# Optimization experiments

Hardware: AMD Instinct MI355X
Metric: run time of the kernel (lower is better)

Reference implementation:

```python
import jax, jax.numpy as jnp
import numpy as np

SCALING_FACTOR = 128.0


def setup_inputs() -> dict:
    key = jax.random.key(0)
    k1, k2, k3, k4 = jax.random.split(key, 4)
    B, G1, G2, DX, DZ, NT = 4, 128, 128, 2, 128, 2048
    x_grid = jax.random.uniform(k1, (B, G1, G2, DX), dtype=jnp.float32)
    z_grid = jax.random.normal(k2, (B, G1, G2, DZ), dtype=jnp.float32)
    xt = jax.random.uniform(k3, (B, NT, DX), dtype=jnp.float32)
    # raw (pre-softplus) lengthscale parameter, one per input dim
    init_ls = 0.1
    lengthscale_param = jnp.full((DX,), np.log(np.exp(init_ls) - 1.0), dtype=jnp.float32)
    lengthscale_param = lengthscale_param + 0.01 * jax.random.normal(k4, (DX,), dtype=jnp.float32)
    return {"x_grid": x_grid, "z_grid": z_grid, "xt": xt, "lengthscale_param": lengthscale_param}


def reference(x_grid, z_grid, xt, lengthscale_param):
    B = x_grid.shape[0]
    dx = x_grid.shape[-1]
    dz = z_grid.shape[-1]
    # flatten spatial grid dims -> (B, ng, d)
    xg = x_grid.reshape(B, -1, dx)
    zg = z_grid.reshape(B, -1, dz)
    # lengthscale = 1e-5 + softplus(param), shape (dx,)
    ls = 1e-5 + jax.nn.softplus(lengthscale_param)
    # pairwise scaled squared distances: (B, nt, ng)
    diff = (xt[:, :, None, :] - xg[:, None, :, :]) / ls  # (B, nt, ng, dx)
    dist2 = jnp.sum(diff * diff, axis=-1)
    weights = jnp.exp(-0.5 * dist2)  # (B, nt, ng)
    # weighted smoothing onto targets
    out = jnp.einsum("btg,bgz->btz", weights, zg) / SCALING_FACTOR
    return out
```

## Files before the change

kernel.cpp:

```cpp
#include <hip/hip_runtime.h>
#include <hip/hip_bf16.h>
#include <cstdint>
#include <cstddef>


typedef float  f32x4  __attribute__((ext_vector_type(4)));
typedef float  f32x16 __attribute__((ext_vector_type(16)));
typedef short  short8 __attribute__((ext_vector_type(8)));
typedef unsigned short ushort4v __attribute__((ext_vector_type(4)));
typedef unsigned short ushort8 __attribute__((ext_vector_type(8)));

#if __has_builtin(__builtin_amdgcn_exp2f)
#define EXP2F(x) __builtin_amdgcn_exp2f(x)
#else
#define EXP2F(x) exp2f(x)
#endif

#define AS1C(p) ((const __attribute__((address_space(1))) void*)(p))
#define AS3(p)  ((__attribute__((address_space(3))) void*)(p))

__device__ __forceinline__ unsigned short bf16_bits(float f) {
  __bf16 h = (__bf16)f;
  return __builtin_bit_cast(unsigned short, h);
}

__global__ __launch_bounds__(256) void pre_kernel(
    const float* __restrict__ x_grid, const float* __restrict__ z_grid,
    const float* __restrict__ xt, const float* __restrict__ lsp,
    unsigned short* __restrict__ zgb, float* __restrict__ xg_trip,
    float* __restrict__ xt4)
{
  __shared__ unsigned short lt[64 * 128];
  const int bid = blockIdx.x;
  const int b   = bid >> 8;
  const int grp = bid & 255;
  const int tid = threadIdx.x;
  const size_t gbase = (size_t)b * 16384 + grp * 64;
  const float sc = 1.0f / 128.0f;

  const float* zr = z_grid + gbase * 128;
  #pragma unroll
  for (int it = 0; it < 8; ++it) {
    const int idx = it * 256 + tid;
    const int row = idx >> 5, c4 = idx & 31;
    f32x4 v = *(const f32x4*)(zr + row * 128 + c4 * 4);
    ushort4v o;
    o.x = bf16_bits(v.x * sc); o.y = bf16_bits(v.y * sc);
    o.z = bf16_bits(v.z * sc); o.w = bf16_bits(v.w * sc);
    *(ushort4v*)(lt + row * 128 + c4 * 4) = o;
  }

  if (tid < 128) {
    const float ls0 = 1e-5f + log1pf(expf(lsp[0]));
    const float ls1 = 1e-5f + log1pf(expf(lsp[1]));
    const float cs  = sqrtf(0.7213475204444817f);
    const float s0 = cs / ls0, s1 = cs / ls1;
    if (tid < 64) {
      const size_t g = gbase + tid;
      const float u0 = x_grid[g * 2 + 0] * s0;
      const float u1 = x_grid[g * 2 + 1] * s1;
      float* d = xg_trip + g * 3;
      d[0] = 2.0f * u0; d[1] = 2.0f * u1; d[2] = -(u0 * u0 + u1 * u1);
    } else if (bid < 128) {
      const int bx = bid >> 5;
      const int r  = (bid & 31) * 64 + (tid - 64);
      const float u0 = xt[((size_t)(bx * 2048 + r)) * 2 + 0] * s0;
      const float u1 = xt[((size_t)(bx * 2048 + r)) * 2 + 1] * s1;
      f32x4 d; d.x = u0; d.y = u1; d.z = -(u0 * u0 + u1 * u1); d.w = 0.0f;
      *(f32x4*)(xt4 + ((size_t)(bx * 2048 + r)) * 4) = d;
    }
  }

  __syncthreads();

  const int q2p = tid >> 7, c = tid & 127;
  #pragma unroll
  for (int h = 0; h < 4; ++h) {
    ushort8 o;
    #pragma unroll
    for (int hi = 0; hi < 2; ++hi)
      #pragma unroll
      for (int j = 0; j < 4; ++j)
        o[hi * 4 + j] = lt[(h * 16 + 4 * q2p + 8 * hi + j) * 128 + c];
    *(ushort8*)(zgb + ((size_t)(b * 1024 + grp * 4 + h)) * 2048
                    + (size_t)(q2p * 128 + c) * 8) = o;
  }
}

__global__ __launch_bounds__(256, 2) void main_kernel(
    const unsigned short* __restrict__ zgb,
    const float* __restrict__ xg_trip,
    const float* __restrict__ xt4,
    float* __restrict__ out,
    float* __restrict__ partials)
{
  __shared__ __align__(128) char smem[65536];
  char* ring = smem;
  char* trip = smem + 24576;

  const int raw = blockIdx.x;
  const int lid = (raw & 7) * 64 + (raw >> 3);
  const int mt  = lid & 15;
  const int b   = (lid >> 4) & 3;
  const int ksp = lid >> 6;

  const int tid = threadIdx.x;
  const int wv  = tid >> 6;
  const int l   = tid & 63;
  const int rh  = wv & 1;
  const int kk  = wv >> 1;
  const int l31 = l & 31;
  const int q2  = l >> 5;
  const int chunk = ksp * 2 + kk;

  float at0[2], at1[2], ca[2];
  #pragma unroll
  for (int mi = 0; mi < 2; ++mi) {
    const int r = mt * 128 + rh * 64 + mi * 32 + l31;
    f32x4 v = *(const f32x4*)(xt4 + ((size_t)(b * 2048 + r)) * 4);
    at0[mi] = v.x; at1[mi] = v.y; ca[mi] = v.z;
  }

  f32x16 acc[2][4];
  #pragma unroll
  for (int mi = 0; mi < 2; ++mi)
    #pragma unroll
    for (int ni = 0; ni < 4; ++ni)
      #pragma unroll
      for (int e = 0; e < 16; ++e)
        acc[mi][ni][e] = 0.0f;

  const char* zsrc = (const char*)zgb + ((size_t)(b * 1024 + chunk * 64)) * 4096;
  const char* tsrc = (const char*)xg_trip + ((size_t)(b * 16384 + ksp * 2048)) * 12;

  auto stage = [&](int s) {
    const char* zs = zsrc + (size_t)s * 4096 + rh * 2048;
    char* zd = ring + (s % 3) * 8192 + kk * 4096 + rh * 2048;
    __builtin_amdgcn_global_load_lds(AS1C(zs + l * 16), AS3(zd + l * 16), 16, 0, 0);
    __builtin_amdgcn_global_load_lds(AS1C(zs + 1024 + l * 16),
                                     AS3(zd + 1024 + l * 16), 16, 0, 0);
  };

  #pragma unroll
  for (int w = 0; w < 6; ++w) {
    const int off = wv * 6144 + w * 1024 + l * 16;
    __builtin_amdgcn_global_load_lds(AS1C(tsrc + off), AS3(trip + off), 16, 0, 0);
  }
  stage(0);
  stage(1);

  #pragma unroll 3
  for (int s = 0; s < 64; ++s) {
    if (s < 63) { asm volatile("s_waitcnt vmcnt(2)" ::: "memory"); }
    else        { asm volatile("s_waitcnt vmcnt(0)" ::: "memory"); }
    __builtin_amdgcn_s_barrier();
    asm volatile("" ::: "memory");

    if (s + 2 < 64) stage(s + 2);

    const float* tb = (const float*)(trip + kk * 12288 + s * 192 + q2 * 48);
    f32x4 L0 = *(const f32x4*)(tb + 0);
    f32x4 L1 = *(const f32x4*)(tb + 4);
    f32x4 L2 = *(const f32x4*)(tb + 8);
    f32x4 H0 = *(const f32x4*)(tb + 24);
    f32x4 H1 = *(const f32x4*)(tb + 28);
    f32x4 H2 = *(const f32x4*)(tb + 32);
    float g0[8], g1[8], cb[8];
    g0[0]=L0.x; g1[0]=L0.y; cb[0]=L0.z;
    g0[1]=L0.w; g1[1]=L1.x; cb[1]=L1.y;
    g0[2]=L1.z; g1[2]=L1.w; cb[2]=L2.x;
    g0[3]=L2.y; g1[3]=L2.z; cb[3]=L2.w;
    g0[4]=H0.x; g1[4]=H0.y; cb[4]=H0.z;
    g0[5]=H0.w; g1[5]=H1.x; cb[5]=H1.y;
    g0[6]=H1.z; g1[6]=H1.w; cb[6]=H2.x;
    g0[7]=H2.y; g1[7]=H2.z; cb[7]=H2.w;

    const char* zt = ring + (s % 3) * 8192 + kk * 4096 + q2 * 2048 + l31 * 16;
    short8 bfr[4];
    #pragma unroll
    for (int ni = 0; ni < 4; ++ni)
      bfr[ni] = *(const short8*)(zt + ni * 512);

    short8 af[2];
    #pragma unroll
    for (int mi = 0; mi < 2; ++mi) {
      union { short8 s8; __bf16 e[8]; } u;
      #pragma unroll
      for (int j = 0; j < 8; ++j) {
        float arg = __builtin_fmaf(at0[mi], g0[j],
                    __builtin_fmaf(at1[mi], g1[j], ca[mi] + cb[j]));
        u.e[j] = (__bf16)EXP2F(arg);
      }
      af[mi] = u.s8;
    }

    #pragma unroll
    for (int mi = 0; mi < 2; ++mi)
      #pragma unroll
      for (int ni = 0; ni < 4; ++ni)
        acc[mi][ni] = __builtin_amdgcn_mfma_f32_32x32x16_bf16(
            af[mi], bfr[ni], acc[mi][ni], 0, 0, 0);
  }

  __syncthreads();
  if (kk == 1) {
    #pragma unroll
    for (int mi = 0; mi < 2; ++mi)
      #pragma unroll
      for (int ni = 0; ni < 4; ++ni)
        #pragma unroll
        for (int q = 0; q < 4; ++q) {
          f32x4 v;
          v.x = acc[mi][ni][q * 4 + 0]; v.y = acc[mi][ni][q * 4 + 1];
          v.z = acc[mi][ni][q * 4 + 2]; v.w = acc[mi][ni][q * 4 + 3];
          *(f32x4*)(smem + rh * 32768 + (mi * 4 + ni) * 4096 + q * 1024 + l * 16) = v;
        }
  }
  __syncthreads();
  if (kk == 0) {
    float* pb = partials ? partials + ((size_t)(ksp * 64 + b * 16 + mt)) * 16384
                         : nullptr;
    #pragma unroll
    for (int mi = 0; mi < 2; ++mi)
      #pragma unroll
      for (int ni = 0; ni < 4; ++ni) {
        #pragma unroll
        for (int q = 0; q < 4; ++q) {
          f32x4 v = *(const f32x4*)(smem + rh * 32768 + (mi * 4 + ni) * 4096
                                         + q * 1024 + l * 16);
          acc[mi][ni][q * 4 + 0] += v.x; acc[mi][ni][q * 4 + 1] += v.y;
          acc[mi][ni][q * 4 + 2] += v.z; acc[mi][ni][q * 4 + 3] += v.w;
        }
        #pragma unroll
        for (int r = 0; r < 16; ++r) {
          const int row = rh * 64 + mi * 32
                        + (r & 3) + 8 * (r >> 2) + 4 * q2;
          const int col = ni * 32 + l31;
          if (pb) {
            pb[row * 128 + col] = acc[mi][ni][r];
          } else {
            atomicAdd(out + ((size_t)b * 2048 + mt * 128 + row) * 128 + col,
                      acc[mi][ni][r]);
          }
        }
      }
  }
}

__global__ __launch_bounds__(256) void reduce_kernel(
    const float* __restrict__ partials, float* __restrict__ out)
{
  const size_t base = ((size_t)blockIdx.x * 256 + threadIdx.x) * 4;
  const float* p = partials + base;
  f32x4 s = *(const f32x4*)p;
  #pragma unroll
  for (int ksv = 1; ksv < 8; ++ksv) {
    f32x4 v = *(const f32x4*)(p + (size_t)ksv * 1048576);
    s.x += v.x; s.y += v.y; s.z += v.z; s.w += v.w;
  }
  *(f32x4*)(out + base) = s;
}

extern "C" void kernel_launch(void* const* d_in, const int* in_sizes, int n_in,
                              void* d_out, int out_size, void* d_ws, size_t ws_size,
                              hipStream_t stream) {
  const float* x_grid = (const float*)d_in[0];
  const float* z_grid = (const float*)d_in[1];
  const float* xt     = (const float*)d_in[2];
  const float* lsp    = (const float*)d_in[3];
  float* out = (float*)d_out;

  char* ws = (char*)d_ws;
  unsigned short* zgb = (unsigned short*)ws;
  float* xg_trip = (float*)(ws + 16777216);
  float* xt4     = (float*)(ws + 16777216 + 786432);
  const size_t poff = 16777216 + 786432 + 131072;
  const bool use_partials = ws_size >= poff + 33554432;
  float* partials = use_partials ? (float*)(ws + poff) : nullptr;

  if (!use_partials)
    hipMemsetAsync(d_out, 0, (size_t)out_size * sizeof(float), stream);
  pre_kernel<<<1024, 256, 0, stream>>>(x_grid, z_grid, xt, lsp,
                                       zgb, xg_trip, xt4);
  main_kernel<<<512, 256, 0, stream>>>(zgb, xg_trip, xt4, out, partials);
  if (use_partials)
    reduce_kernel<<<1024, 256, 0, stream>>>(partials, out);
}
```

Baseline: 140.8 us.

## Double K-step per barrier, load grid triples directly into registers, split reduction

Each pipeline stage now covers two 16-wide K sub-steps using a 4-deep LDS ring, so the loop runs 32 barriers instead of 64. The grid coordinate triples are no longer staged in LDS. They are loaded from global memory straight into double-buffered registers one step ahead. The cross-wave reduction is split per mi, which halves its LDS footprint at the cost of extra syncthreads. The changes aim to cut barrier and LDS traffic overhead, in exchange for higher register pressure that could hurt occupancy at the 2-blocks bound.

```diff
diff --git a/kernel.cpp b/kernel.cpp
--- a/kernel.cpp
+++ b/kernel.cpp
@@ -95,8 +95,6 @@
     float* __restrict__ partials)
 {
   __shared__ __align__(128) char smem[65536];
-  char* ring = smem;
-  char* trip = smem + 24576;
 
   const int raw = blockIdx.x;
   const int lid = (raw & 7) * 64 + (raw >> 3);
@@ -131,81 +129,111 @@
         acc[mi][ni][e] = 0.0f;
 
   const char* zsrc = (const char*)zgb + ((size_t)(b * 1024 + chunk * 64)) * 4096;
-  const char* tsrc = (const char*)xg_trip + ((size_t)(b * 16384 + ksp * 2048)) * 12;
+  const char* tsrc = (const char*)xg_trip
+                   + ((size_t)(b * 16384 + chunk * 1024)) * 12 + q2 * 48;
 
   auto stage = [&](int s) {
-    const char* zs = zsrc + (size_t)s * 4096 + rh * 2048;
-    char* zd = ring + (s % 3) * 8192 + kk * 4096 + rh * 2048;
+    const char* zs = zsrc + (size_t)s * 8192 + rh * 2048;
+    char* zd = smem + (s & 3) * 16384 + kk * 8192 + rh * 2048;
     __builtin_amdgcn_global_load_lds(AS1C(zs + l * 16), AS3(zd + l * 16), 16, 0, 0);
     __builtin_amdgcn_global_load_lds(AS1C(zs + 1024 + l * 16),
                                      AS3(zd + 1024 + l * 16), 16, 0, 0);
+    __builtin_amdgcn_global_load_lds(AS1C(zs + 4096 + l * 16),
+                                     AS3(zd + 4096 + l * 16), 16, 0, 0);
+    __builtin_amdgcn_global_load_lds(AS1C(zs + 5120 + l * 16),
+                                     AS3(zd + 5120 + l * 16), 16, 0, 0);
   };
 
-  #pragma unroll
-  for (int w = 0; w < 6; ++w) {
-    const int off = wv * 6144 + w * 1024 + l * 16;
-    __builtin_amdgcn_global_load_lds(AS1C(tsrc + off), AS3(trip + off), 16, 0, 0);
-  }
-  stage(0);
-  stage(1);
-
-  #pragma unroll 3
-  for (int s = 0; s < 64; ++s) {
-    if (s < 63) { asm volatile("s_waitcnt vmcnt(2)" ::: "memory"); }
-    else        { asm volatile("s_waitcnt vmcnt(0)" ::: "memory"); }
-    __builtin_amdgcn_s_barrier();
-    asm volatile("" ::: "memory");
-
-    if (s + 2 < 64) stage(s + 2);
-
-    const float* tb = (const float*)(trip + kk * 12288 + s * 192 + q2 * 48);
-    f32x4 L0 = *(const f32x4*)(tb + 0);
-    f32x4 L1 = *(const f32x4*)(tb + 4);
-    f32x4 L2 = *(const f32x4*)(tb + 8);
-    f32x4 H0 = *(const f32x4*)(tb + 24);
-    f32x4 H1 = *(const f32x4*)(tb + 28);
-    f32x4 H2 = *(const f32x4*)(tb + 32);
-    float g0[8], g1[8], cb[8];
-    g0[0]=L0.x; g1[0]=L0.y; cb[0]=L0.z;
-    g0[1]=L0.w; g1[1]=L1.x; cb[1]=L1.y;
-    g0[2]=L1.z; g1[2]=L1.w; cb[2]=L2.x;
-    g0[3]=L2.y; g1[3]=L2.z; cb[3]=L2.w;
-    g0[4]=H0.x; g1[4]=H0.y; cb[4]=H0.z;
-    g0[5]=H0.w; g1[5]=H1.x; cb[5]=H1.y;
-    g0[6]=H1.z; g1[6]=H1.w; cb[6]=H2.x;
-    g0[7]=H2.y; g1[7]=H2.z; cb[7]=H2.w;
-
-    const char* zt = ring + (s % 3) * 8192 + kk * 4096 + q2 * 2048 + l31 * 16;
-    short8 bfr[4];
+  auto loadT = [&](int s, f32x4* T) {
+    const char* tp = tsrc + (size_t)s * 384;
+    T[0]  = *(const f32x4*)(tp + 0);
+    T[1]  = *(const f32x4*)(tp + 16);
+    T[2]  = *(const f32x4*)(tp + 32);
+    T[3]  = *(const f32x4*)(tp + 96);
+    T[4]  = *(const f32x4*)(tp + 112);
+    T[5]  = *(const f32x4*)(tp + 128);
+    T[6]  = *(const f32x4*)(tp + 192);
+    T[7]  = *(const f32x4*)(tp + 208);
+    T[8]  = *(const f32x4*)(tp + 224);
+    T[9]  = *(const f32x4*)(tp + 288);
+    T[10] = *(const f32x4*)(tp + 304);
+    T[11] = *(const f32x4*)(tp + 320);
+  };
+
+  auto computeIter = [&](int s, const f32x4* T) {
     #pragma unroll
-    for (int ni = 0; ni < 4; ++ni)
-      bfr[ni] = *(const short8*)(zt + ni * 512);
-
-    short8 af[2];
-    #pragma unroll
-    for (int mi = 0; mi < 2; ++mi) {
-      union { short8 s8; __bf16 e[8]; } u;
-      #pragma unroll
-      for (int j = 0; j < 8; ++j) {
-        float arg = __builtin_fmaf(at0[mi], g0[j],
-                    __builtin_fmaf(at1[mi], g1[j], ca[mi] + cb[j]));
-        u.e[j] = (__bf16)EXP2F(arg);
+    for (int sub = 0; sub < 2; ++sub) {
+      const f32x4 L0 = T[sub * 6 + 0], L1 = T[sub * 6 + 1], L2 = T[sub * 6 + 2];
+      const f32x4 H0 = T[sub * 6 + 3], H1 = T[sub * 6 + 4], H2 = T[sub * 6 + 5];
+      float g0[8], g1[8], cb[8];
+      g0[0]=L0.x; g1[0]=L0.y; cb[0]=L0.z;
+      g0[1]=L0.w; g1[1]=L1.x; cb[1]=L1.y;
+      g0[2]=L1.z; g1[2]=L1.w; cb[2]=L2.x;
+      g0[3]=L2.y; g1[3]=L2.z; cb[3]=L2.w;
+      g0[4]=H0.x; g1[4]=H0.y; cb[4]=H0.z;
+      g0[5]=H0.w; g1[5]=H1.x; cb[5]=H1.y;
+      g0[6]=H1.z; g1[6]=H1.w; cb[6]=H2.x;
+      g0[7]=H2.y; g1[7]=H2.z; cb[7]=H2.w;
+
+      const char* zt = smem + (s & 3) * 16384 + kk * 8192 + sub * 4096
+                     + q2 * 2048 + l31 * 16;
+      short8 bfr[4];
+      #pragma unroll
+      for (int ni = 0; ni < 4; ++ni)
+        bfr[ni] = *(const short8*)(zt + ni * 512);
+
+      short8 af[2];
+      #pragma unroll
+      for (int mi = 0; mi < 2; ++mi) {
+        union { short8 s8; __bf16 e[8]; } u;
+        #pragma unroll
+        for (int j = 0; j < 8; ++j) {
+          float arg = __builtin_fmaf(at0[mi], g0[j],
+                      __builtin_fmaf(at1[mi], g1[j], ca[mi] + cb[j]));
+          u.e[j] = (__bf16)EXP2F(arg);
+        }
+        af[mi] = u.s8;
       }
-      af[mi] = u.s8;
-    }
-
-    #pragma unroll
-    for (int mi = 0; mi < 2; ++mi)
-      #pragma unroll
-      for (int ni = 0; ni < 4; ++ni)
-        acc[mi][ni] = __builtin_amdgcn_mfma_f32_32x32x16_bf16(
-            af[mi], bfr[ni], acc[mi][ni], 0, 0, 0);
+
+      #pragma unroll
+      for (int mi = 0; mi < 2; ++mi)
+        #pragma unroll
+        for (int ni = 0; ni < 4; ++ni)
+          acc[mi][ni] = __builtin_amdgcn_mfma_f32_32x32x16_bf16(
+              af[mi], bfr[ni], acc[mi][ni], 0, 0, 0);
+    }
+  };
+
+  f32x4 TA[12], TB[12];
+  stage(0); loadT(0, TA); stage(1);
+
+  for (int i = 0; i < 16; ++i) {
+    { const int s = 2 * i;
+      asm volatile("s_waitcnt vmcnt(4)" ::: "memory");
+      __builtin_amdgcn_s_barrier();
+      asm volatile("" ::: "memory");
+      loadT(s + 1, TB);
+      if (s + 2 < 32) stage(s + 2);
+      computeIter(s, TA);
+    }
+    { const int s = 2 * i + 1;
+      if (s < 31) { asm volatile("s_waitcnt vmcnt(4)" ::: "memory"); }
+      else        { asm volatile("s_waitcnt vmcnt(0)" ::: "memory"); }
+      __builtin_amdgcn_s_barrier();
+      asm volatile("" ::: "memory");
+      if (s + 1 < 32) loadT(s + 1, TA);
+      if (s + 2 < 32) stage(s + 2);
+      computeIter(s, TB);
+    }
   }
 
   __syncthreads();
-  if (kk == 1) {
-    #pragma unroll
-    for (int mi = 0; mi < 2; ++mi)
+  float* red = (float*)smem;
+  float* pb = partials ? partials + ((size_t)(ksp * 64 + b * 16 + mt)) * 16384
+                       : nullptr;
+  #pragma unroll
+  for (int mi = 0; mi < 2; ++mi) {
+    if (kk == 1) {
       #pragma unroll
       for (int ni = 0; ni < 4; ++ni)
         #pragma unroll
@@ -213,21 +241,16 @@
           f32x4 v;
           v.x = acc[mi][ni][q * 4 + 0]; v.y = acc[mi][ni][q * 4 + 1];
           v.z = acc[mi][ni][q * 4 + 2]; v.w = acc[mi][ni][q * 4 + 3];
-          *(f32x4*)(smem + rh * 32768 + (mi * 4 + ni) * 4096 + q * 1024 + l * 16) = v;
+          *(f32x4*)(red + rh * 4096 + ni * 1024 + q * 256 + l * 4) = v;
         }
-  }
-  __syncthreads();
-  if (kk == 0) {
-    float* pb = partials ? partials + ((size_t)(ksp * 64 + b * 16 + mt)) * 16384
-                         : nullptr;
-    #pragma unroll
-    for (int mi = 0; mi < 2; ++mi)
+    }
+    __syncthreads();
+    if (kk == 0) {
       #pragma unroll
       for (int ni = 0; ni < 4; ++ni) {
         #pragma unroll
         for (int q = 0; q < 4; ++q) {
-          f32x4 v = *(const f32x4*)(smem + rh * 32768 + (mi * 4 + ni) * 4096
-                                         + q * 1024 + l * 16);
+          f32x4 v = *(const f32x4*)(red + rh * 4096 + ni * 1024 + q * 256 + l * 4);
           acc[mi][ni][q * 4 + 0] += v.x; acc[mi][ni][q * 4 + 1] += v.y;
           acc[mi][ni][q * 4 + 2] += v.z; acc[mi][ni][q * 4 + 3] += v.w;
         }
@@ -244,6 +267,8 @@
           }
         }
       }
+    }
+    __syncthreads();
   }
 }
 
```

Result: slower. 144.3 us (+2.5%).
